# Kernel tuning notes

Measured on AMD Instinct MI355X. Metric: run time of the kernel, lower is better.

Reference implementation:

```python
import jax, jax.numpy as jnp
import numpy as np

B, N, D = 4, 1024, 1024
H = 16
HD = D // H
FF = int(D * 2.0)
EPS = 1e-5


def setup_inputs() -> dict:
    key = jax.random.key(0)
    ks = jax.random.split(key, 12)
    s = lambda fan_in: 1.0 / np.sqrt(fan_in)
    return {
        "x": jax.random.normal(ks[0], (B, N, D), dtype=jnp.float32),
        "ln1_g": jnp.ones((D,), jnp.float32),
        "ln1_b": jnp.zeros((D,), jnp.float32),
        "qkv_w": jax.random.normal(ks[1], (D, 3 * D), jnp.float32) * s(D),
        "qkv_b": jnp.zeros((3 * D,), jnp.float32),
        "out_w": jax.random.normal(ks[2], (D, D), jnp.float32) * s(D),
        "out_b": jnp.zeros((D,), jnp.float32),
        "ln2_g": jnp.ones((D,), jnp.float32),
        "ln2_b": jnp.zeros((D,), jnp.float32),
        "w1": jax.random.normal(ks[3], (D, FF), jnp.float32) * s(D),
        "b1": jnp.zeros((FF,), jnp.float32),
        "w2": jax.random.normal(ks[4], (FF, D), jnp.float32) * s(FF),
        "b2": jnp.zeros((D,), jnp.float32),
    }


def _layernorm(x, g, b):
    mu = jnp.mean(x, axis=-1, keepdims=True)
    var = jnp.mean(jnp.square(x - mu), axis=-1, keepdims=True)
    return (x - mu) * jax.lax.rsqrt(var + EPS) * g + b


def _attention(x, qkv_w, qkv_b, out_w, out_b):
    qkv = x @ qkv_w + qkv_b                       # (B,N,3D)
    qkv = qkv.reshape(B, N, 3, H, HD)
    q, k, v = qkv[:, :, 0], qkv[:, :, 1], qkv[:, :, 2]  # (B,N,H,HD)
    scale = 1.0 / np.sqrt(HD)
    attn = jnp.einsum("bnhd,bmhd->bhnm", q, k) * scale
    attn = jax.nn.softmax(attn, axis=-1)
    out = jnp.einsum("bhnm,bmhd->bnhd", attn, v).reshape(B, N, D)
    return out @ out_w + out_b


def reference(x, ln1_g, ln1_b, qkv_w, qkv_b, out_w, out_b, ln2_g, ln2_b, w1, b1, w2, b2):
    x = x + _attention(_layernorm(x, ln1_g, ln1_b), qkv_w, qkv_b, out_w, out_b)
    h = _layernorm(x, ln2_g, ln2_b)
    h = jax.nn.gelu(h @ w1 + b1, approximate=False) @ w2 + b2
    return x + h
```

## Files before the change

kernel.cpp:

```cpp
#include <hip/hip_runtime.h>
#include <hip/hip_bf16.h>
#include <cstdint>
#include <cstddef>

#define Bq 4
#define Nseq 1024
#define Dm 1024
#define Hh 16
#define HDd 64
#define FFd 2048
#define Mrows 4096

typedef __attribute__((ext_vector_type(8))) short bf16x8;
typedef __attribute__((ext_vector_type(4))) float f32x4;
typedef __attribute__((ext_vector_type(16))) float f32x16;

__device__ __forceinline__ void gl_lds16(const void* g, void* l) {
  __builtin_amdgcn_global_load_lds(
      (const __attribute__((address_space(1))) unsigned int*)g,
      (__attribute__((address_space(3))) unsigned int*)l, 16, 0, 0);
}

__device__ __forceinline__ unsigned short f2b(float f) {
  union { __hip_bfloat16 h; unsigned short u; } cv;
  cv.h = __float2bfloat16(f);
  return cv.u;
}

__device__ __forceinline__ unsigned cvt_pk_bf16(float a, float b) {
  unsigned r;
  asm("v_cvt_pk_bf16_f32 %0, %1, %2" : "=v"(r) : "v"(a), "v"(b));
  return r;
}

__device__ __forceinline__ void pl32_swap(unsigned& a, unsigned& b) {
  asm("v_permlane32_swap_b32 %0, %1" : "+v"(a), "+v"(b));
}

__device__ __forceinline__ int xcd_swz(int d, int nwg) {
  return (d & 7) * (nwg >> 3) + (d >> 3);
}

__device__ __forceinline__ void tr_tile(const float* __restrict__ src,
                                        __hip_bfloat16* __restrict__ dst,
                                        int K, int Ncols, int n0, int k0,
                                        int tid) {
  __shared__ float tile[32][33];
  const int tx = tid & 31, ty = tid >> 5;
#pragma unroll
  for (int i = 0; i < 32; i += 8)
    tile[ty + i][tx] = src[(size_t)(k0 + ty + i) * Ncols + n0 + tx];
  __syncthreads();
#pragma unroll
  for (int i = 0; i < 32; i += 8)
    dst[(size_t)(n0 + ty + i) * K + k0 + tx] = __float2bfloat16(tile[tx][ty + i]);
}

__global__ __launch_bounds__(256) void prep_kernel(
    const float* __restrict__ qkv_w, __hip_bfloat16* __restrict__ wqkv_t,
    const float* __restrict__ out_w, __hip_bfloat16* __restrict__ wout_t,
    const float* __restrict__ w1, __hip_bfloat16* __restrict__ w1_t,
    const float* __restrict__ w2, __hip_bfloat16* __restrict__ w2_t,
    const float* __restrict__ x, const float* __restrict__ ln1_g,
    const float* __restrict__ ln1_b, __hip_bfloat16* __restrict__ xn) {
  const int id = blockIdx.x, tid = threadIdx.x;
  if (id < 3072) {
    tr_tile(qkv_w, wqkv_t, Dm, 3 * Dm, (id % 96) * 32, (id / 96) * 32, tid);
  } else if (id < 4096) {
    const int i2 = id - 3072;
    tr_tile(out_w, wout_t, Dm, Dm, (i2 % 32) * 32, (i2 / 32) * 32, tid);
  } else if (id < 6144) {
    const int i2 = id - 4096;
    tr_tile(w1, w1_t, Dm, FFd, (i2 % 64) * 32, (i2 / 64) * 32, tid);
  } else if (id < 8192) {
    const int i2 = id - 6144;
    tr_tile(w2, w2_t, FFd, Dm, (i2 % 32) * 32, (i2 / 32) * 32, tid);
  } else {
    const int row = id - 8192;
    const float4 v = reinterpret_cast<const float4*>(x + (size_t)row * Dm)[tid];
    float s1 = v.x + v.y + v.z + v.w;
    float s2 = v.x * v.x + v.y * v.y + v.z * v.z + v.w * v.w;
#pragma unroll
    for (int m = 1; m < 64; m <<= 1) {
      s1 += __shfl_xor(s1, m);
      s2 += __shfl_xor(s2, m);
    }
    __shared__ float a1[4], a2[4];
    const int wv = tid >> 6;
    if ((tid & 63) == 0) { a1[wv] = s1; a2[wv] = s2; }
    __syncthreads();
    s1 = a1[0] + a1[1] + a1[2] + a1[3];
    s2 = a2[0] + a2[1] + a2[2] + a2[3];
    const float mu = s1 * (1.f / Dm);
    const float rs = rsqrtf(s2 * (1.f / Dm) - mu * mu + 1e-5f);
    const float4 g4 = reinterpret_cast<const float4*>(ln1_g)[tid];
    const float4 b4 = reinterpret_cast<const float4*>(ln1_b)[tid];
    ushort4 o;
    o.x = f2b((v.x - mu) * rs * g4.x + b4.x);
    o.y = f2b((v.y - mu) * rs * g4.y + b4.y);
    o.z = f2b((v.z - mu) * rs * g4.z + b4.z);
    o.w = f2b((v.w - mu) * rs * g4.w + b4.w);
    reinterpret_cast<ushort4*>(xn + (size_t)row * Dm)[tid] = o;
  }
}

__global__ __launch_bounds__(256) void ln_bf16_kernel(
    const __hip_bfloat16* __restrict__ xb, const float* __restrict__ gw,
    const float* __restrict__ bw, __hip_bfloat16* __restrict__ out) {
  const int row = blockIdx.x;
  const ushort4 u = reinterpret_cast<const ushort4*>(xb + (size_t)row * Dm)[threadIdx.x];
  union { __hip_bfloat16 h; unsigned short s; } c0{{}}, c1{{}}, c2{{}}, c3{{}};
  c0.s = u.x; c1.s = u.y; c2.s = u.z; c3.s = u.w;
  float vx = __bfloat162float(c0.h), vy = __bfloat162float(c1.h);
  float vz = __bfloat162float(c2.h), vw = __bfloat162float(c3.h);
  float s1 = vx + vy + vz + vw;
  float s2 = vx * vx + vy * vy + vz * vz + vw * vw;
#pragma unroll
  for (int m = 1; m < 64; m <<= 1) {
    s1 += __shfl_xor(s1, m);
    s2 += __shfl_xor(s2, m);
  }
  __shared__ float a1[4], a2[4];
  const int wv = threadIdx.x >> 6;
  if ((threadIdx.x & 63) == 0) { a1[wv] = s1; a2[wv] = s2; }
  __syncthreads();
  s1 = a1[0] + a1[1] + a1[2] + a1[3];
  s2 = a2[0] + a2[1] + a2[2] + a2[3];
  const float mu = s1 * (1.f / Dm);
  const float rs = rsqrtf(s2 * (1.f / Dm) - mu * mu + 1e-5f);
  const float4 g4 = reinterpret_cast<const float4*>(gw)[threadIdx.x];
  const float4 b4 = reinterpret_cast<const float4*>(bw)[threadIdx.x];
  ushort4 o;
  o.x = f2b((vx - mu) * rs * g4.x + b4.x);
  o.y = f2b((vy - mu) * rs * g4.y + b4.y);
  o.z = f2b((vz - mu) * rs * g4.z + b4.z);
  o.w = f2b((vw - mu) * rs * g4.w + b4.w);
  reinterpret_cast<ushort4*>(out + (size_t)row * Dm)[threadIdx.x] = o;
}

__global__ __launch_bounds__(256, 3) void gemm_qkv(
    const __hip_bfloat16* __restrict__ A, const __hip_bfloat16* __restrict__ BT,
    const float* __restrict__ bias,
    __hip_bfloat16* __restrict__ qb, __hip_bfloat16* __restrict__ kb,
    __hip_bfloat16* __restrict__ vtb, int Ndim, int Kdim) {
  __shared__ alignas(16) __hip_bfloat16 As[128 * 64];
  __shared__ alignas(16) __hip_bfloat16 Bs[128 * 64];
  const int tid = threadIdx.x;
  const int wv = tid >> 6, ln = tid & 63;
  const int wm = wv >> 1, wn = wv & 1;
  const int lq = ln & 31, hl = ln >> 5;
  const int gx = gridDim.x;
  const int l = xcd_swz(blockIdx.x + gx * blockIdx.y, gx * gridDim.y);
  const int rowBase = (l / gx) * 128;
  const int colBase = (l % gx) * 128;

  const int st_row = tid >> 3;
  const int st_c = (tid & 7) ^ (st_row & 7);

  f32x16 acc[2][2];
#pragma unroll
  for (int i = 0; i < 2; ++i)
#pragma unroll
    for (int j = 0; j < 2; ++j) acc[i][j] = {};

  auto stage = [&](int k0) {
#pragma unroll
    for (int r = 0; r < 4; ++r) {
      gl_lds16(A + (size_t)(rowBase + r * 32 + st_row) * Kdim + k0 + st_c * 8,
               (char*)As + r * 4096 + wv * 1024);
      gl_lds16(BT + (size_t)(colBase + r * 32 + st_row) * Kdim + k0 + st_c * 8,
               (char*)Bs + r * 4096 + wv * 1024);
    }
  };

  const int nt = Kdim >> 6;
  for (int kt = 0; kt < nt; ++kt) {
    stage(kt << 6);
    __syncthreads();
    const char* Ap = (const char*)As;
    const char* Bp = (const char*)Bs;
#pragma unroll
    for (int ks = 0; ks < 4; ++ks) {
      bf16x8 af[2], bfr[2];
#pragma unroll
      for (int i = 0; i < 2; ++i)
        af[i] = *reinterpret_cast<const bf16x8*>(
            Ap + (wm * 64 + i * 32 + lq) * 128 + (((ks * 2 + hl) ^ (lq & 7)) * 16));
#pragma unroll
      for (int j = 0; j < 2; ++j)
        bfr[j] = *reinterpret_cast<const bf16x8*>(
            Bp + (wn * 64 + j * 32 + lq) * 128 + (((ks * 2 + hl) ^ (lq & 7)) * 16));
#pragma unroll
      for (int i = 0; i < 2; ++i)
#pragma unroll
        for (int j = 0; j < 2; ++j)
          acc[i][j] = __builtin_amdgcn_mfma_f32_32x32x16_bf16(af[i], bfr[j], acc[i][j], 0, 0, 0);
    }
    __syncthreads();
  }

#pragma unroll
  for (int i = 0; i < 2; ++i) {
#pragma unroll
    for (int j = 0; j < 2; ++j) {
      const int gc = colBase + wn * 64 + j * 32 + lq;
      const float bv = bias[gc];
#pragma unroll
      for (int r = 0; r < 16; ++r) {
        const int gr = rowBase + wm * 64 + i * 32 + (r & 3) + 8 * (r >> 2) + 4 * hl;
        float v = acc[i][j][r] + bv;
        const int which = gc >> 10;
        const int dcol = gc & 1023;
        const int h = dcol >> 6, hd = dcol & 63;
        const int b = gr >> 10, n = gr & 1023;
        const size_t bh = (size_t)(b * Hh + h);
        if (which == 0)
          qb[(bh * Nseq + n) * HDd + hd] = __float2bfloat16(v * 0.125f);
        else if (which == 1)
          kb[(bh * Nseq + n) * HDd + hd] = __float2bfloat16(v);
        else
          vtb[(bh * HDd + hd) * Nseq + n] = __float2bfloat16(v);
      }
    }
  }
}

template <int EPI>
__global__ __launch_bounds__(256, 4) void gemm_sk(
    const __hip_bfloat16* __restrict__ A, const __hip_bfloat16* __restrict__ BT,
    const float* __restrict__ bias, const float* __restrict__ resF,
    const __hip_bfloat16* __restrict__ resB,
    float* __restrict__ outF, __hip_bfloat16* __restrict__ outB,
    int Ndim, int Kdim) {
  __shared__ alignas(16) __hip_bfloat16 As[64 * 64];
  __shared__ alignas(16) __hip_bfloat16 Bs[128 * 64];
  const int tid = threadIdx.x;
  const int wv = tid >> 6, ln = tid & 63;
  const int wm = wv >> 1, wn = wv & 1;
  const int lq = ln & 31, hl = ln >> 5;
  const int gx = gridDim.x;
  const int l = xcd_swz(blockIdx.x + gx * blockIdx.y, gx * gridDim.y);
  const int rowBase = (l / gx) * 64;
  const int colBase = (l % gx) * 128;

  const int st_row = tid >> 3;
  const int st_c = (tid & 7) ^ (st_row & 7);

  f32x16 acc[2];
  acc[0] = {}; acc[1] = {};

  auto stage = [&](int k0) {
#pragma unroll
    for (int r = 0; r < 2; ++r)
      gl_lds16(A + (size_t)(rowBase + r * 32 + st_row) * Kdim + k0 + st_c * 8,
               (char*)As + r * 4096 + wv * 1024);
#pragma unroll
    for (int r = 0; r < 4; ++r)
      gl_lds16(BT + (size_t)(colBase + r * 32 + st_row) * Kdim + k0 + st_c * 8,
               (char*)Bs + r * 4096 + wv * 1024);
  };

  const int nt = Kdim >> 6;
  for (int kt = 0; kt < nt; ++kt) {
    stage(kt << 6);
    __syncthreads();
    const char* Ap = (const char*)As;
    const char* Bp = (const char*)Bs;
#pragma unroll
    for (int ks = 0; ks < 4; ++ks) {
      const int csw = ((ks * 2 + hl) ^ (lq & 7)) * 16;
      const bf16x8 af = *reinterpret_cast<const bf16x8*>(
          Ap + (wm * 32 + lq) * 128 + csw);
#pragma unroll
      for (int j = 0; j < 2; ++j) {
        const bf16x8 bfr = *reinterpret_cast<const bf16x8*>(
            Bp + (wn * 64 + j * 32 + lq) * 128 + csw);
        acc[j] = __builtin_amdgcn_mfma_f32_32x32x16_bf16(af, bfr, acc[j], 0, 0, 0);
      }
    }
    __syncthreads();
  }

#pragma unroll
  for (int j = 0; j < 2; ++j) {
    const int gc = colBase + wn * 64 + j * 32 + lq;
    const float bv = bias[gc];
#pragma unroll
    for (int r = 0; r < 16; ++r) {
      const int gr = rowBase + wm * 32 + (r & 3) + 8 * (r >> 2) + 4 * hl;
      const float v = acc[j][r] + bv;
      if constexpr (EPI == 1) {
        outB[(size_t)gr * Ndim + gc] =
            __float2bfloat16(v + resF[(size_t)gr * Ndim + gc]);
      } else if constexpr (EPI == 2) {
        outB[(size_t)gr * Ndim + gc] =
            __float2bfloat16(0.5f * v * (1.f + erff(v * 0.70710678118f)));
      } else {
        outF[(size_t)gr * Ndim + gc] =
            v + __bfloat162float(resB[(size_t)gr * Ndim + gc]);
      }
    }
  }
}

__global__ __launch_bounds__(256, 2) void attn_kernel(
    const __hip_bfloat16* __restrict__ q, const __hip_bfloat16* __restrict__ k,
    const __hip_bfloat16* __restrict__ vt, __hip_bfloat16* __restrict__ attn) {
  __shared__ alignas(16) __hip_bfloat16 Ks[2][128 * 64];
  __shared__ alignas(16) __hip_bfloat16 Vs[2][64 * 128];
  const int tid = threadIdx.x, wv = tid >> 6, ln = tid & 63;
  const int l = xcd_swz(blockIdx.x, gridDim.x);
  const int bh = l >> 3, qt = l & 7;
  const int b = bh >> 4, h = bh & 15;
  const int lq = ln & 31;
  const int hl = ln >> 5;

  const __hip_bfloat16* kbase = k + (size_t)bh * Nseq * HDd;
  const __hip_bfloat16* vbase = vt + (size_t)bh * HDd * Nseq;

  const int st_r = ln >> 3;
  const int st_c = (ln & 7) ^ st_r;
  const int sv_r = ln >> 4;
  const int sv_ci = ln & 15;

  const __hip_bfloat16* qsrc = q + ((size_t)bh * Nseq + qt * 128 + wv * 32 + lq) * HDd;
  bf16x8 qf[4];
#pragma unroll
  for (int s = 0; s < 4; ++s)
    qf[s] = *reinterpret_cast<const bf16x8*>(qsrc + s * 16 + hl * 8);

  float mrun = -1e30f, lrun = 0.f;
  f32x16 ot0 = {}, ot1 = {};

  auto stage = [&](int buf, int kt) {
#pragma unroll
    for (int c = 0; c < 4; ++c) {
      const int kc = wv * 4 + c;
      gl_lds16(kbase + ((size_t)kt * 128 + kc * 8 + st_r) * HDd + st_c * 8,
               (char*)&Ks[buf][0] + kc * 1024);
      const int vr = kc * 4 + sv_r;
      gl_lds16(vbase + (size_t)vr * Nseq + kt * 128 + (sv_ci ^ (vr & 7)) * 8,
               (char*)&Vs[buf][0] + kc * 1024);
    }
  };

  stage(0, 0);
  __syncthreads();
  int cur = 0;

  for (int kt = 0; kt < 8; ++kt) {
    if (kt < 7) stage(cur ^ 1, kt + 1);

    const char* Kp = (const char*)&Ks[cur][0];
    const char* Vp = (const char*)&Vs[cur][0];

    f32x16 st0 = {}, st1 = {}, st2 = {}, st3 = {};
#pragma unroll
    for (int t = 0; t < 4; ++t) {
      const int row = t * 32 + lq;
#pragma unroll
      for (int s = 0; s < 4; ++s) {
        const bf16x8 kf = *reinterpret_cast<const bf16x8*>(
            Kp + row * 128 + (((s * 2 + hl) ^ (row & 7)) * 16));
        if (t == 0)      st0 = __builtin_amdgcn_mfma_f32_32x32x16_bf16(kf, qf[s], st0, 0, 0, 0);
        else if (t == 1) st1 = __builtin_amdgcn_mfma_f32_32x32x16_bf16(kf, qf[s], st1, 0, 0, 0);
        else if (t == 2) st2 = __builtin_amdgcn_mfma_f32_32x32x16_bf16(kf, qf[s], st2, 0, 0, 0);
        else             st3 = __builtin_amdgcn_mfma_f32_32x32x16_bf16(kf, qf[s], st3, 0, 0, 0);
      }
    }

    float tmax = st0[0];
#pragma unroll
    for (int r = 1; r < 16; ++r) tmax = fmaxf(tmax, st0[r]);
#pragma unroll
    for (int r = 0; r < 16; ++r) tmax = fmaxf(tmax, st1[r]);
#pragma unroll
    for (int r = 0; r < 16; ++r) tmax = fmaxf(tmax, st2[r]);
#pragma unroll
    for (int r = 0; r < 16; ++r) tmax = fmaxf(tmax, st3[r]);
    tmax = fmaxf(tmax, __shfl_xor(tmax, 32));
    const float mn = fmaxf(mrun, tmax);
    const float sc = __expf(mrun - mn);
    mrun = mn;
    float tsum = 0.f;
#pragma unroll
    for (int r = 0; r < 16; ++r) { st0[r] = __expf(st0[r] - mn); tsum += st0[r]; }
#pragma unroll
    for (int r = 0; r < 16; ++r) { st1[r] = __expf(st1[r] - mn); tsum += st1[r]; }
#pragma unroll
    for (int r = 0; r < 16; ++r) { st2[r] = __expf(st2[r] - mn); tsum += st2[r]; }
#pragma unroll
    for (int r = 0; r < 16; ++r) { st3[r] = __expf(st3[r] - mn); tsum += st3[r]; }
    tsum += __shfl_xor(tsum, 32);
    lrun = lrun * sc + tsum;
#pragma unroll
    for (int r = 0; r < 16; ++r) { ot0[r] *= sc; ot1[r] *= sc; }

    union PF { unsigned u[4]; bf16x8 v; } pf[8];
#pragma unroll
    for (int t = 0; t < 4; ++t)
#pragma unroll
      for (int g = 0; g < 2; ++g) {
        float p0, p1, p2, p3, p4, p5, p6, p7;
        if (t == 0) { p0 = st0[g*8+0]; p1 = st0[g*8+1]; p2 = st0[g*8+2]; p3 = st0[g*8+3];
                      p4 = st0[g*8+4]; p5 = st0[g*8+5]; p6 = st0[g*8+6]; p7 = st0[g*8+7]; }
        else if (t == 1) { p0 = st1[g*8+0]; p1 = st1[g*8+1]; p2 = st1[g*8+2]; p3 = st1[g*8+3];
                           p4 = st1[g*8+4]; p5 = st1[g*8+5]; p6 = st1[g*8+6]; p7 = st1[g*8+7]; }
        else if (t == 2) { p0 = st2[g*8+0]; p1 = st2[g*8+1]; p2 = st2[g*8+2]; p3 = st2[g*8+3];
                           p4 = st2[g*8+4]; p5 = st2[g*8+5]; p6 = st2[g*8+6]; p7 = st2[g*8+7]; }
        else { p0 = st3[g*8+0]; p1 = st3[g*8+1]; p2 = st3[g*8+2]; p3 = st3[g*8+3];
               p4 = st3[g*8+4]; p5 = st3[g*8+5]; p6 = st3[g*8+6]; p7 = st3[g*8+7]; }
        unsigned w0 = cvt_pk_bf16(p0, p1);
        unsigned w1 = cvt_pk_bf16(p2, p3);
        unsigned w2 = cvt_pk_bf16(p4, p5);
        unsigned w3 = cvt_pk_bf16(p6, p7);
        pl32_swap(w0, w2);
        pl32_swap(w1, w3);
        PF f;
        f.u[0] = w0; f.u[1] = w1; f.u[2] = w2; f.u[3] = w3;
        pf[t * 2 + g] = f;
      }

#pragma unroll
    for (int dt = 0; dt < 2; ++dt) {
      const int row = dt * 32 + lq;
#pragma unroll
      for (int ks = 0; ks < 8; ++ks) {
        const bf16x8 vf = *reinterpret_cast<const bf16x8*>(
            Vp + row * 256 + (((ks * 2 + hl) ^ (row & 7)) * 16));
        if (dt == 0) ot0 = __builtin_amdgcn_mfma_f32_32x32x16_bf16(vf, pf[ks].v, ot0, 0, 0, 0);
        else         ot1 = __builtin_amdgcn_mfma_f32_32x32x16_bf16(vf, pf[ks].v, ot1, 0, 0, 0);
      }
    }

    __syncthreads();
    cur ^= 1;
  }

  const float inv = 1.f / lrun;
  char* swb = (char*)(&Ks[0][0] + wv * 2048);
#pragma unroll
  for (int dt = 0; dt < 2; ++dt)
#pragma unroll
    for (int i = 0; i < 8; ++i) {
      const unsigned w = (dt == 0)
          ? cvt_pk_bf16(ot0[2 * i] * inv, ot0[2 * i + 1] * inv)
          : cvt_pk_bf16(ot1[2 * i] * inv, ot1[2 * i + 1] * inv);
      const int d0 = (2 * i & 2) + 8 * (i >> 1) + 4 * hl + 32 * dt;
      *(unsigned*)(swb + lq * 128 + (((d0 >> 3) ^ (lq & 7)) * 16) + (d0 & 7) * 2) = w;
    }
  const int brow = b * Nseq + qt * 128 + wv * 32;
#pragma unroll
  for (int it = 0; it < 4; ++it) {
    const int qr = it * 8 + (ln >> 3);
    const bf16x8 o = *reinterpret_cast<const bf16x8*>(
        swb + qr * 128 + (((ln & 7) ^ (qr & 7)) * 16));
    *reinterpret_cast<bf16x8*>(attn + (size_t)(brow + qr) * Dm + h * 64 + (ln & 7) * 8) = o;
  }
}

extern "C" void kernel_launch(void* const* d_in, const int* in_sizes, int n_in,
                              void* d_out, int out_size, void* d_ws, size_t ws_size,
                              hipStream_t stream) {
  (void)in_sizes; (void)n_in; (void)out_size; (void)ws_size;
  const float* x     = (const float*)d_in[0];
  const float* ln1_g = (const float*)d_in[1];
  const float* ln1_b = (const float*)d_in[2];
  const float* qkv_w = (const float*)d_in[3];
  const float* qkv_b = (const float*)d_in[4];
  const float* out_w = (const float*)d_in[5];
  const float* out_b = (const float*)d_in[6];
  const float* ln2_g = (const float*)d_in[7];
  const float* ln2_b = (const float*)d_in[8];
  const float* w1    = (const float*)d_in[9];
  const float* b1    = (const float*)d_in[10];
  const float* w2    = (const float*)d_in[11];
  const float* b2    = (const float*)d_in[12];
  float* outp = (float*)d_out;

  char* ws = (char*)d_ws;
  size_t off = 0;
  auto take = [&](size_t bytes) {
    char* p = ws + off;
    off += (bytes + 255) & ~(size_t)255;
    return p;
  };
  __hip_bfloat16* wqkv_t = (__hip_bfloat16*)take((size_t)3 * Dm * Dm * 2);
  __hip_bfloat16* wout_t = (__hip_bfloat16*)take((size_t)Dm * Dm * 2);
  __hip_bfloat16* w1_t   = (__hip_bfloat16*)take((size_t)FFd * Dm * 2);
  __hip_bfloat16* w2_t   = (__hip_bfloat16*)take((size_t)Dm * FFd * 2);
  __hip_bfloat16* xn     = (__hip_bfloat16*)take((size_t)Mrows * Dm * 2);
  __hip_bfloat16* qb     = (__hip_bfloat16*)take((size_t)Mrows * Dm * 2);
  __hip_bfloat16* kb     = (__hip_bfloat16*)take((size_t)Mrows * Dm * 2);
  __hip_bfloat16* vtb    = (__hip_bfloat16*)take((size_t)Mrows * Dm * 2);
  __hip_bfloat16* attn   = (__hip_bfloat16*)take((size_t)Mrows * Dm * 2);
  __hip_bfloat16* x1b    = (__hip_bfloat16*)take((size_t)Mrows * Dm * 2);
  __hip_bfloat16* gbuf   = (__hip_bfloat16*)take((size_t)Mrows * FFd * 2);

  const dim3 blk(256);
  prep_kernel<<<dim3(12288), blk, 0, stream>>>(
      qkv_w, wqkv_t, out_w, wout_t, w1, w1_t, w2, w2_t, x, ln1_g, ln1_b, xn);
  gemm_qkv<<<dim3(3 * Dm / 128, Mrows / 128), blk, 0, stream>>>(
      xn, wqkv_t, qkv_b, qb, kb, vtb, 3 * Dm, Dm);
  attn_kernel<<<dim3(Bq * Hh * (Nseq / 128)), blk, 0, stream>>>(qb, kb, vtb, attn);
  gemm_sk<1><<<dim3(Dm / 128, Mrows / 64), blk, 0, stream>>>(
      attn, wout_t, out_b, x, nullptr, nullptr, x1b, Dm, Dm);
  ln_bf16_kernel<<<dim3(Mrows), blk, 0, stream>>>(x1b, ln2_g, ln2_b, xn);
  gemm_sk<2><<<dim3(FFd / 128, Mrows / 64), blk, 0, stream>>>(
      xn, w1_t, b1, nullptr, nullptr, nullptr, gbuf, FFd, Dm);
  gemm_sk<3><<<dim3(Dm / 128, Mrows / 64), blk, 0, stream>>>(
      gbuf, w2_t, b2, nullptr, x1b, outp, nullptr, Dm, FFd);
}
```

Baseline: 166.6 us.

## Double-buffer QKV GEMM LDS tiles with async prefetch two steps ahead

The QKV projection GEMM now splits its LDS staging into two 32-wide K buffers and issues global-to-LDS loads for step kt+2 while computing step kt, using explicit vmcnt waits and barriers instead of a load-then-sync per 64-wide tile. The swizzle pattern is changed to match the narrower 64-byte rows. This aims to hide global load latency behind MFMA work. In exchange it doubles the number of loop iterations and barriers, and the hand-written waitcnt logic is fragile.

Measured after the change: 170.7 us. 1.02x slower.

```diff
diff --git a/kernel.cpp b/kernel.cpp
--- a/kernel.cpp
+++ b/kernel.cpp
@@ -143,8 +143,8 @@
     const float* __restrict__ bias,
     __hip_bfloat16* __restrict__ qb, __hip_bfloat16* __restrict__ kb,
     __hip_bfloat16* __restrict__ vtb, int Ndim, int Kdim) {
-  __shared__ alignas(16) __hip_bfloat16 As[128 * 64];
-  __shared__ alignas(16) __hip_bfloat16 Bs[128 * 64];
+  __shared__ alignas(16) __hip_bfloat16 As[2][128 * 32];
+  __shared__ alignas(16) __hip_bfloat16 Bs[2][128 * 32];
   const int tid = threadIdx.x;
   const int wv = tid >> 6, ln = tid & 63;
   const int wm = wv >> 1, wn = wv & 1;
@@ -154,8 +154,9 @@
   const int rowBase = (l / gx) * 128;
   const int colBase = (l % gx) * 128;
 
-  const int st_row = tid >> 3;
-  const int st_c = (tid & 7) ^ (st_row & 7);
+  const int st_row = wv * 16 + (ln >> 2);
+  const int st_lc  = (ln & 3) ^ ((ln >> 3) & 3);
+  const int rsw    = (lq >> 1) & 3;
 
   f32x16 acc[2][2];
 #pragma unroll
@@ -163,40 +164,52 @@
 #pragma unroll
     for (int j = 0; j < 2; ++j) acc[i][j] = {};
 
-  auto stage = [&](int k0) {
-#pragma unroll
-    for (int r = 0; r < 4; ++r) {
-      gl_lds16(A + (size_t)(rowBase + r * 32 + st_row) * Kdim + k0 + st_c * 8,
-               (char*)As + r * 4096 + wv * 1024);
-      gl_lds16(BT + (size_t)(colBase + r * 32 + st_row) * Kdim + k0 + st_c * 8,
-               (char*)Bs + r * 4096 + wv * 1024);
+  auto stage = [&](int buf, int k0) {
+#pragma unroll
+    for (int r = 0; r < 2; ++r) {
+      gl_lds16(A + (size_t)(rowBase + r * 64 + st_row) * Kdim + k0 + st_lc * 8,
+               (char*)&As[buf][0] + r * 4096 + wv * 1024);
+      gl_lds16(BT + (size_t)(colBase + r * 64 + st_row) * Kdim + k0 + st_lc * 8,
+               (char*)&Bs[buf][0] + r * 4096 + wv * 1024);
     }
   };
 
-  const int nt = Kdim >> 6;
+  const int nt = Kdim >> 5;
+  stage(0, 0);
+  stage(1, 32);
+  asm volatile("s_waitcnt vmcnt(4)" ::: "memory");
+  __builtin_amdgcn_s_barrier();
+
   for (int kt = 0; kt < nt; ++kt) {
-    stage(kt << 6);
-    __syncthreads();
-    const char* Ap = (const char*)As;
-    const char* Bp = (const char*)Bs;
-#pragma unroll
-    for (int ks = 0; ks < 4; ++ks) {
+    const char* Ap = (const char*)&As[kt & 1][0];
+    const char* Bp = (const char*)&Bs[kt & 1][0];
+#pragma unroll
+    for (int ks = 0; ks < 2; ++ks) {
       bf16x8 af[2], bfr[2];
 #pragma unroll
       for (int i = 0; i < 2; ++i)
         af[i] = *reinterpret_cast<const bf16x8*>(
-            Ap + (wm * 64 + i * 32 + lq) * 128 + (((ks * 2 + hl) ^ (lq & 7)) * 16));
+            Ap + (wm * 64 + i * 32 + lq) * 64 + (((ks * 2 + hl) ^ rsw) * 16));
 #pragma unroll
       for (int j = 0; j < 2; ++j)
         bfr[j] = *reinterpret_cast<const bf16x8*>(
-            Bp + (wn * 64 + j * 32 + lq) * 128 + (((ks * 2 + hl) ^ (lq & 7)) * 16));
+            Bp + (wn * 64 + j * 32 + lq) * 64 + (((ks * 2 + hl) ^ rsw) * 16));
 #pragma unroll
       for (int i = 0; i < 2; ++i)
 #pragma unroll
         for (int j = 0; j < 2; ++j)
           acc[i][j] = __builtin_amdgcn_mfma_f32_32x32x16_bf16(af[i], bfr[j], acc[i][j], 0, 0, 0);
     }
-    __syncthreads();
+    if (kt + 1 < nt) {
+      __builtin_amdgcn_s_barrier();
+      if (kt + 2 < nt) {
+        stage(kt & 1, (kt + 2) << 5);
+        asm volatile("s_waitcnt vmcnt(4)" ::: "memory");
+      } else {
+        asm volatile("s_waitcnt vmcnt(0)" ::: "memory");
+      }
+      __builtin_amdgcn_s_barrier();
+    }
   }
 
 #pragma unroll
```
